# Performance work log

Hardware: AMD Instinct MI355X
Metric: run time of the kernel (lower is better)

The kernel has to match this reference:

```python
import jax, jax.numpy as jnp
import numpy as np

B, N, E = 16, 5000, 160000
IN, OUT, H = 64, 64, 1  # heads=1 (GATConv default)
NEG_SLOPE = 0.2


def setup_inputs() -> dict:
    key = jax.random.key(0)
    ks = jax.random.split(key, 10)
    data = jax.random.normal(ks[0], (B, N, IN), jnp.float32)
    # random edges with no self-loops (PyG removes then re-adds self-loops;
    # with no pre-existing self-loops this matches exactly)
    src = jax.random.randint(ks[1], (E,), 0, N)
    off = jax.random.randint(ks[2], (E,), 1, N)
    dst = (src + off) % N
    edge_index = jnp.stack([src, dst]).astype(jnp.int32)
    edge_attr = jax.random.uniform(ks[3], (E,), jnp.float32)
    # GATConv parameters (glorot-ish init)
    W = jax.random.normal(ks[4], (H * OUT, IN), jnp.float32) / np.sqrt(IN)
    W_edge = jax.random.normal(ks[5], (H * OUT, 1), jnp.float32)
    att_src = jax.random.normal(ks[6], (1, H, OUT), jnp.float32) * 0.1
    att_dst = jax.random.normal(ks[7], (1, H, OUT), jnp.float32) * 0.1
    att_edge = jax.random.normal(ks[8], (1, H, OUT), jnp.float32) * 0.1
    bias = jnp.zeros((H * OUT,), jnp.float32)
    return {"data": data, "edge_index": edge_index, "edge_attr": edge_attr,
            "W": W, "W_edge": W_edge, "att_src": att_src, "att_dst": att_dst,
            "att_edge": att_edge, "bias": bias}


def reference(data, edge_index, edge_attr, W, W_edge, att_src, att_dst, att_edge, bias):
    BN = B * N
    x = data.reshape(BN, IN)
    # faithful to source: tile edges per batch WITHOUT node offset
    ei = jnp.tile(edge_index, (1, B))          # [2, B*E]
    ea = jnp.tile(edge_attr, B)[:, None]        # [B*E, 1]
    # add self-loops for all BN nodes, edge_attr filled with mean
    loops = jnp.arange(BN, dtype=ei.dtype)
    src = jnp.concatenate([ei[0], loops])       # [Etot]
    dst = jnp.concatenate([ei[1], loops])
    ea = jnp.concatenate([ea, jnp.full((BN, 1), ea.mean(), ea.dtype)])
    # linear transforms
    xl = (x @ W.T).reshape(BN, H, OUT)          # [BN, H, C]
    a_src = (xl * att_src).sum(-1)              # [BN, H]
    a_dst = (xl * att_dst).sum(-1)
    e_emb = (ea @ W_edge.T).reshape(-1, H, OUT) # [Etot, H, C]
    a_edge = (e_emb * att_edge).sum(-1)         # [Etot, H]
    # per-edge attention + segment softmax over destination nodes
    alpha = a_src[src] + a_dst[dst] + a_edge
    alpha = jax.nn.leaky_relu(alpha, NEG_SLOPE)
    amax = jax.ops.segment_max(alpha, dst, num_segments=BN)
    alpha = jnp.exp(alpha - amax[dst])
    denom = jax.ops.segment_sum(alpha, dst, num_segments=BN)
    alpha = alpha / (denom[dst] + 1e-16)
    # message passing: gather src features, weight, scatter-sum to dst
    msg = xl[src] * alpha[:, :, None]           # [Etot, H, C]
    out = jax.ops.segment_sum(msg, dst, num_segments=BN)
    out = out.reshape(BN, H * OUT) + bias
    return out.reshape(B, N, OUT), jnp.stack([src, dst]), alpha
```

## Files before the change

kernel.cpp:

```cpp
#include <hip/hip_runtime.h>

#define NN 5000
#define EE 160000
#define BNN 80000
#define BEE 2560000
#define ETOT 2640000
#define CAP 128
#define POISON ((int)0xAAAAAAAA)

#define FILL_BLKS 625
#define GEMM_BLKS 1250
#define SUM_BLKS  80
#define MEGA_BLKS (FILL_BLKS + GEMM_BLKS + SUM_BLKS)

#define K3_BLKS 2578

typedef __attribute__((ext_vector_type(8))) short short8;
typedef __attribute__((ext_vector_type(4))) float floatx4;

__device__ __forceinline__ short8 pack_bf8(const float* p) {
    union { unsigned int u[4]; short8 s; } r;
    #pragma unroll
    for (int j = 0; j < 4; ++j) {
        unsigned int lo = __float_as_uint(p[2 * j]) >> 16;
        unsigned int hi = __float_as_uint(p[2 * j + 1]) & 0xFFFF0000u;
        r.u[j] = lo | hi;
    }
    return r.s;
}

__device__ __forceinline__ void nt_store4(float a, float b, float c, float d, float* p) {
    floatx4 v = {a, b, c, d};
    __builtin_nontemporal_store(v, reinterpret_cast<floatx4*>(p));
}

__global__ __launch_bounds__(256) void k_mega(
        const float* __restrict__ x, const float* __restrict__ W,
        const float* __restrict__ att_src, const float* __restrict__ att_dst,
        const float* __restrict__ bias,
        const float* __restrict__ ea, const float* __restrict__ wedge,
        const float* __restrict__ atte, const int* __restrict__ ei,
        float* __restrict__ xl, float* __restrict__ asrc, float* __restrict__ adst,
        float* __restrict__ out0,
        int* __restrict__ cursor, int* __restrict__ bucket, float* __restrict__ eabuf,
        float* __restrict__ partials) {
    __shared__ float red[256];
    const int blk = blockIdx.x;
    const int t = threadIdx.x;

    if (blk < FILL_BLKS) {
        int e = blk * 256 + t;
        int s = ei[e];
        int d = ei[EE + e];
        float ev = ea[e];
        int pos = atomicAdd(&cursor[d], 1) - POISON;
        if (pos < CAP) {
            bucket[d * CAP + pos] = (s << 18) | e;
            eabuf[d * CAP + pos] = ev;
        }
    } else if (blk < FILL_BLKS + GEMM_BLKS) {
        const int gblk = blk - FILL_BLKS;
        const int wave = t >> 6;
        const int lane = t & 63;
        const int quad = lane >> 4;
        const int col  = lane & 15;
        short8 bfrag[4][2];
        float attsv[4], attdv[4], biasv[4];
        #pragma unroll
        for (int ct = 0; ct < 4; ++ct) {
            int c = ct * 16 + col;
            #pragma unroll
            for (int ks = 0; ks < 2; ++ks)
                bfrag[ct][ks] = pack_bf8(W + c * 64 + ks * 32 + quad * 8);
            attsv[ct] = att_src[c];
            attdv[ct] = att_dst[c];
            biasv[ct] = bias[c];
        }
        int node0 = (gblk * 4 + wave) << 4;
        short8 afrag[2];
        const float* xrow = x + (size_t)(node0 + col) * 64;
        #pragma unroll
        for (int ks = 0; ks < 2; ++ks)
            afrag[ks] = pack_bf8(xrow + ks * 32 + quad * 8);
        floatx4 acc[4];
        #pragma unroll
        for (int ct = 0; ct < 4; ++ct) acc[ct] = (floatx4){0.f, 0.f, 0.f, 0.f};
        #pragma unroll
        for (int ks = 0; ks < 2; ++ks)
            #pragma unroll
            for (int ct = 0; ct < 4; ++ct)
                acc[ct] = __builtin_amdgcn_mfma_f32_16x16x32_bf16(afrag[ks], bfrag[ct][ks], acc[ct], 0, 0, 0);
        float ps[4] = {0.f,0.f,0.f,0.f}, pd[4] = {0.f,0.f,0.f,0.f};
        #pragma unroll
        for (int r = 0; r < 4; ++r) {
            int node = node0 + quad * 4 + r;
            #pragma unroll
            for (int ct = 0; ct < 4; ++ct) {
                float v = acc[ct][r];
                if (node < NN) xl[node * 64 + ct * 16 + col] = v;
                else           out0[node * 64 + ct * 16 + col] = v + biasv[ct];
                ps[r] += v * attsv[ct];
                pd[r] += v * attdv[ct];
            }
        }
        if (node0 < NN) {
            #pragma unroll
            for (int off = 1; off < 16; off <<= 1) {
                #pragma unroll
                for (int r = 0; r < 4; ++r) {
                    ps[r] += __shfl_xor(ps[r], off, 64);
                    pd[r] += __shfl_xor(pd[r], off, 64);
                }
            }
            if (col == 0) {
                #pragma unroll
                for (int r = 0; r < 4; ++r) {
                    int node = node0 + quad * 4 + r;
                    if (node < NN) { asrc[node] = ps[r]; adst[node] = pd[r]; }
                }
            }
        }
    } else {
        int sb = blk - (FILL_BLKS + GEMM_BLKS);
        int gid = sb * 256 + t;
        float v = 0.f;
        for (int i = gid; i < EE; i += SUM_BLKS * 256) v += ea[i];
        red[t] = v;
        __syncthreads();
        #pragma unroll
        for (int off = 128; off > 0; off >>= 1) {
            if (t < off) red[t] += red[t + off];
            __syncthreads();
        }
        if (t == 0) partials[sb] = red[0];
        if (sb == 0 && t < 64) {
            float s = wedge[t] * atte[t];
            #pragma unroll
            for (int off = 32; off > 0; off >>= 1) s += __shfl_xor(s, off, 64);
            if (t == 0) partials[80] = s;
        }
    }
}

__global__ __launch_bounds__(256) void k_gather(
        const int* __restrict__ bucket, const float* __restrict__ eabuf,
        const int* __restrict__ cursor,
        const float* __restrict__ asrc, const float* __restrict__ adst,
        const float* __restrict__ partials,
        const float* __restrict__ xl, const float* __restrict__ bias,
        float* __restrict__ albuf, float* __restrict__ selfal,
        float* __restrict__ out0) {
    __shared__ float s_w[4][CAP];
    __shared__ int   s_se[4][CAP];
    __shared__ int   s_e[4][CAP];
    const int t = threadIdx.x, w = t >> 6, lane = t & 63;
    float s0 = 0.f;
    #pragma unroll
    for (int i = 0; i < 80; ++i) s0 += partials[i];
    float s1 = partials[80];
    float selfadd = s0 * (1.0f / EE) * s1;
    float bl = bias[lane];
    int d = blockIdx.x * 4 + w;
    float* sw = s_w[w]; int* sse = s_se[w]; int* se_ = s_e[w];
    int deg = min(cursor[d] - POISON, CAP);
    float ad = adst[d];
    float rs = asrc[d] + ad + selfadd;
    rs = (rs > 0.f) ? rs : 0.2f * rs;
    float es = __expf(rs);
    for (int base = 0; base < deg; base += 64) {
        int idx = base + lane;
        if (idx < deg) {
            int packed = bucket[d * CAP + idx];
            float ev   = eabuf[d * CAP + idx];
            int se = packed >> 18;
            int e  = packed & 0x3FFFF;
            float r = asrc[se] + ad + ev * s1;
            r = (r > 0.f) ? r : 0.2f * r;
            sw[idx] = __expf(r); sse[idx] = se; se_[idx] = e;
        }
    }
    float l = es;
    float acc = es * xl[d * 64 + lane];
    int j = 0;
    for (; j + 4 <= deg; j += 4) {
        int a0 = sse[j], a1 = sse[j + 1], a2 = sse[j + 2], a3 = sse[j + 3];
        float x0 = xl[a0 * 64 + lane], x1 = xl[a1 * 64 + lane];
        float x2 = xl[a2 * 64 + lane], x3 = xl[a3 * 64 + lane];
        float w0 = sw[j], w1 = sw[j + 1], w2 = sw[j + 2], w3 = sw[j + 3];
        acc += 16.0f * (w0 * x0 + w1 * x1 + w2 * x2 + w3 * x3);
        l   += 16.0f * (w0 + w1 + w2 + w3);
    }
    for (; j < deg; ++j) {
        acc += 16.0f * sw[j] * xl[sse[j] * 64 + lane];
        l   += 16.0f * sw[j];
    }
    float inv = 1.0f / (l + 1e-16f);
    out0[d * 64 + lane] = acc * inv + bl;
    if (lane == 0) selfal[d] = es * inv;
    for (int idx = lane; idx < deg; idx += 64)
        albuf[se_[idx]] = sw[idx] * inv;
}

__global__ __launch_bounds__(256) void k3(
        const int* __restrict__ ei,
        const float* __restrict__ albuf, const float* __restrict__ selfal,
        float* __restrict__ out1, float* __restrict__ out2) {
    for (int q = blockIdx.x * 256 + threadIdx.x; q < ETOT / 4; q += K3_BLKS * 256) {
        int i = q * 4;
        if (i < BEE) {
            int oe = i % EE;
            int4 s4 = *reinterpret_cast<const int4*>(ei + oe);
            int4 d4 = *reinterpret_cast<const int4*>(ei + EE + oe);
            nt_store4((float)s4.x, (float)s4.y, (float)s4.z, (float)s4.w, out1 + i);
            nt_store4((float)d4.x, (float)d4.y, (float)d4.z, (float)d4.w, out1 + ETOT + i);
            float4 av = *reinterpret_cast<const float4*>(albuf + oe);
            nt_store4(av.x, av.y, av.z, av.w, out2 + i);
        } else {
            int nn = i - BEE;
            nt_store4((float)nn, (float)(nn+1), (float)(nn+2), (float)(nn+3), out1 + i);
            nt_store4((float)nn, (float)(nn+1), (float)(nn+2), (float)(nn+3), out1 + ETOT + i);
            float a[4];
            #pragma unroll
            for (int jj = 0; jj < 4; ++jj) {
                int v = nn + jj;
                a[jj] = (v < NN) ? selfal[v] : 1.0f;
            }
            nt_store4(a[0], a[1], a[2], a[3], out2 + i);
        }
    }
}

extern "C" void kernel_launch(void* const* d_in, const int* in_sizes, int n_in,
                              void* d_out, int out_size, void* d_ws, size_t ws_size,
                              hipStream_t stream) {
    const float* data  = (const float*)d_in[0];
    const int*   ei    = (const int*)d_in[1];
    const float* ea    = (const float*)d_in[2];
    const float* W     = (const float*)d_in[3];
    const float* wedge = (const float*)d_in[4];
    const float* atts  = (const float*)d_in[5];
    const float* attd  = (const float*)d_in[6];
    const float* atte  = (const float*)d_in[7];
    const float* bias  = (const float*)d_in[8];

    float* out0 = (float*)d_out;
    float* out1 = out0 + 5120000;
    float* out2 = out0 + 10400000;

    float* ws = (float*)d_ws;
    float* xl       = ws;
    float* asrc     = ws + 320000;
    float* adst     = ws + 325000;
    float* albuf    = ws + 330000;
    float* selfal   = ws + 490000;
    float* partials = ws + 495000;
    int*   cursor   = (int*)(ws + 495082);
    int*   bucket   = (int*)(ws + 500082);
    float* eabuf    = ws + 1140082;

    k_mega  <<<MEGA_BLKS, 256, 0, stream>>>(data, W, atts, attd, bias, ea, wedge,
                                            atte, ei, xl, asrc, adst, out0,
                                            cursor, bucket, eabuf, partials);
    k_gather<<<1250,      256, 0, stream>>>(bucket, eabuf, cursor, asrc, adst,
                                            partials, xl, bias, albuf, selfal, out0);
    k3      <<<K3_BLKS,   256, 0, stream>>>(ei, albuf, selfal, out1, out2);
}
```

Measured before the change: 125.6 us.

## Move edge-index output writes into gather kernel to overlap with gather work

The out1 writes (src/dst index conversion to float), which do not depend on attention results, move out of the final kernel. They now run in extra blocks appended to the gather kernel, so their store bandwidth overlaps the latency-bound gather. The final kernel writes only the alpha output. This trades a lighter tail kernel for a larger grid in the gather launch, whose extra blocks may compete with gather blocks for CUs and bandwidth.

```diff
diff --git a/kernel.cpp b/kernel.cpp
--- a/kernel.cpp
+++ b/kernel.cpp
@@ -13,7 +13,11 @@
 #define SUM_BLKS  80
 #define MEGA_BLKS (FILL_BLKS + GEMM_BLKS + SUM_BLKS)
 
-#define K3_BLKS 2578
+#define KB_GATHER 1250
+#define KB_OUT1   2578
+#define KB_BLKS   (KB_GATHER + KB_OUT1)
+
+#define KC_BLKS 2578
 
 typedef __attribute__((ext_vector_type(8))) short short8;
 typedef __attribute__((ext_vector_type(4))) float floatx4;
@@ -142,83 +146,96 @@
     }
 }
 
-__global__ __launch_bounds__(256) void k_gather(
+__global__ __launch_bounds__(256) void k_B(
+        const int* __restrict__ ei,
         const int* __restrict__ bucket, const float* __restrict__ eabuf,
         const int* __restrict__ cursor,
         const float* __restrict__ asrc, const float* __restrict__ adst,
         const float* __restrict__ partials,
         const float* __restrict__ xl, const float* __restrict__ bias,
         float* __restrict__ albuf, float* __restrict__ selfal,
-        float* __restrict__ out0) {
+        float* __restrict__ out0, float* __restrict__ out1) {
     __shared__ float s_w[4][CAP];
     __shared__ int   s_se[4][CAP];
     __shared__ int   s_e[4][CAP];
+    const int blk = blockIdx.x;
     const int t = threadIdx.x, w = t >> 6, lane = t & 63;
-    float s0 = 0.f;
-    #pragma unroll
-    for (int i = 0; i < 80; ++i) s0 += partials[i];
-    float s1 = partials[80];
-    float selfadd = s0 * (1.0f / EE) * s1;
-    float bl = bias[lane];
-    int d = blockIdx.x * 4 + w;
-    float* sw = s_w[w]; int* sse = s_se[w]; int* se_ = s_e[w];
-    int deg = min(cursor[d] - POISON, CAP);
-    float ad = adst[d];
-    float rs = asrc[d] + ad + selfadd;
-    rs = (rs > 0.f) ? rs : 0.2f * rs;
-    float es = __expf(rs);
-    for (int base = 0; base < deg; base += 64) {
-        int idx = base + lane;
-        if (idx < deg) {
-            int packed = bucket[d * CAP + idx];
-            float ev   = eabuf[d * CAP + idx];
-            int se = packed >> 18;
-            int e  = packed & 0x3FFFF;
-            float r = asrc[se] + ad + ev * s1;
-            r = (r > 0.f) ? r : 0.2f * r;
-            sw[idx] = __expf(r); sse[idx] = se; se_[idx] = e;
-        }
-    }
-    float l = es;
-    float acc = es * xl[d * 64 + lane];
-    int j = 0;
-    for (; j + 4 <= deg; j += 4) {
-        int a0 = sse[j], a1 = sse[j + 1], a2 = sse[j + 2], a3 = sse[j + 3];
-        float x0 = xl[a0 * 64 + lane], x1 = xl[a1 * 64 + lane];
-        float x2 = xl[a2 * 64 + lane], x3 = xl[a3 * 64 + lane];
-        float w0 = sw[j], w1 = sw[j + 1], w2 = sw[j + 2], w3 = sw[j + 3];
-        acc += 16.0f * (w0 * x0 + w1 * x1 + w2 * x2 + w3 * x3);
-        l   += 16.0f * (w0 + w1 + w2 + w3);
-    }
-    for (; j < deg; ++j) {
-        acc += 16.0f * sw[j] * xl[sse[j] * 64 + lane];
-        l   += 16.0f * sw[j];
-    }
-    float inv = 1.0f / (l + 1e-16f);
-    out0[d * 64 + lane] = acc * inv + bl;
-    if (lane == 0) selfal[d] = es * inv;
-    for (int idx = lane; idx < deg; idx += 64)
-        albuf[se_[idx]] = sw[idx] * inv;
-}
-
-__global__ __launch_bounds__(256) void k3(
-        const int* __restrict__ ei,
+
+    if (blk < KB_GATHER) {
+        float s0 = 0.f;
+        #pragma unroll
+        for (int i = 0; i < 80; ++i) s0 += partials[i];
+        float s1 = partials[80];
+        float selfadd = s0 * (1.0f / EE) * s1;
+        float bl = bias[lane];
+        int d = blk * 4 + w;
+        float* sw = s_w[w]; int* sse = s_se[w]; int* se_ = s_e[w];
+        int deg = min(cursor[d] - POISON, CAP);
+        float ad = adst[d];
+        float rs = asrc[d] + ad + selfadd;
+        rs = (rs > 0.f) ? rs : 0.2f * rs;
+        float es = __expf(rs);
+        for (int base = 0; base < deg; base += 64) {
+            int idx = base + lane;
+            if (idx < deg) {
+                int packed = bucket[d * CAP + idx];
+                float ev   = eabuf[d * CAP + idx];
+                int se = packed >> 18;
+                int e  = packed & 0x3FFFF;
+                float r = asrc[se] + ad + ev * s1;
+                r = (r > 0.f) ? r : 0.2f * r;
+                sw[idx] = __expf(r); sse[idx] = se; se_[idx] = e;
+            }
+        }
+        float l = es;
+        float acc = es * xl[d * 64 + lane];
+        int j = 0;
+        for (; j + 4 <= deg; j += 4) {
+            int a0 = sse[j], a1 = sse[j + 1], a2 = sse[j + 2], a3 = sse[j + 3];
+            float x0 = xl[a0 * 64 + lane], x1 = xl[a1 * 64 + lane];
+            float x2 = xl[a2 * 64 + lane], x3 = xl[a3 * 64 + lane];
+            float w0 = sw[j], w1 = sw[j + 1], w2 = sw[j + 2], w3 = sw[j + 3];
+            acc += 16.0f * (w0 * x0 + w1 * x1 + w2 * x2 + w3 * x3);
+            l   += 16.0f * (w0 + w1 + w2 + w3);
+        }
+        for (; j < deg; ++j) {
+            acc += 16.0f * sw[j] * xl[sse[j] * 64 + lane];
+            l   += 16.0f * sw[j];
+        }
+        float inv = 1.0f / (l + 1e-16f);
+        out0[d * 64 + lane] = acc * inv + bl;
+        if (lane == 0) selfal[d] = es * inv;
+        for (int idx = lane; idx < deg; idx += 64)
+            albuf[se_[idx]] = sw[idx] * inv;
+    } else {
+        int qb = blk - KB_GATHER;
+        for (int q = qb * 256 + t; q < ETOT / 4; q += KB_OUT1 * 256) {
+            int i = q * 4;
+            if (i < BEE) {
+                int oe = i % EE;
+                int4 s4 = *reinterpret_cast<const int4*>(ei + oe);
+                int4 d4 = *reinterpret_cast<const int4*>(ei + EE + oe);
+                nt_store4((float)s4.x, (float)s4.y, (float)s4.z, (float)s4.w, out1 + i);
+                nt_store4((float)d4.x, (float)d4.y, (float)d4.z, (float)d4.w, out1 + ETOT + i);
+            } else {
+                int nn = i - BEE;
+                nt_store4((float)nn, (float)(nn+1), (float)(nn+2), (float)(nn+3), out1 + i);
+                nt_store4((float)nn, (float)(nn+1), (float)(nn+2), (float)(nn+3), out1 + ETOT + i);
+            }
+        }
+    }
+}
+
+__global__ __launch_bounds__(256) void k_C(
         const float* __restrict__ albuf, const float* __restrict__ selfal,
-        float* __restrict__ out1, float* __restrict__ out2) {
-    for (int q = blockIdx.x * 256 + threadIdx.x; q < ETOT / 4; q += K3_BLKS * 256) {
+        float* __restrict__ out2) {
+    for (int q = blockIdx.x * 256 + threadIdx.x; q < ETOT / 4; q += KC_BLKS * 256) {
         int i = q * 4;
         if (i < BEE) {
-            int oe = i % EE;
-            int4 s4 = *reinterpret_cast<const int4*>(ei + oe);
-            int4 d4 = *reinterpret_cast<const int4*>(ei + EE + oe);
-            nt_store4((float)s4.x, (float)s4.y, (float)s4.z, (float)s4.w, out1 + i);
-            nt_store4((float)d4.x, (float)d4.y, (float)d4.z, (float)d4.w, out1 + ETOT + i);
-            float4 av = *reinterpret_cast<const float4*>(albuf + oe);
+            float4 av = *reinterpret_cast<const float4*>(albuf + (i % EE));
             nt_store4(av.x, av.y, av.z, av.w, out2 + i);
         } else {
             int nn = i - BEE;
-            nt_store4((float)nn, (float)(nn+1), (float)(nn+2), (float)(nn+3), out1 + i);
-            nt_store4((float)nn, (float)(nn+1), (float)(nn+2), (float)(nn+3), out1 + ETOT + i);
             float a[4];
             #pragma unroll
             for (int jj = 0; jj < 4; ++jj) {
@@ -258,10 +275,11 @@
     int*   bucket   = (int*)(ws + 500082);
     float* eabuf    = ws + 1140082;
 
-    k_mega  <<<MEGA_BLKS, 256, 0, stream>>>(data, W, atts, attd, bias, ea, wedge,
-                                            atte, ei, xl, asrc, adst, out0,
-                                            cursor, bucket, eabuf, partials);
-    k_gather<<<1250,      256, 0, stream>>>(bucket, eabuf, cursor, asrc, adst,
-                                            partials, xl, bias, albuf, selfal, out0);
-    k3      <<<K3_BLKS,   256, 0, stream>>>(ei, albuf, selfal, out1, out2);
-}
+    k_mega<<<MEGA_BLKS, 256, 0, stream>>>(data, W, atts, attd, bias, ea, wedge,
+                                          atte, ei, xl, asrc, adst, out0,
+                                          cursor, bucket, eabuf, partials);
+    k_B   <<<KB_BLKS,   256, 0, stream>>>(ei, bucket, eabuf, cursor, asrc, adst,
+                                          partials, xl, bias, albuf, selfal,
+                                          out0, out1);
+    k_C   <<<KC_BLKS,   256, 0, stream>>>(albuf, selfal, out2);
+}
```

Result: no change. 126.1 us (+0.4%).
